# Kernel tuning notes

Measured on AMD Instinct MI355X. Metric: run time of the kernel, lower is better.

The kernel has to match this reference:

```python
import jax, jax.numpy as jnp
import numpy as np

B, L, C1, C2, K, K_IN = 4, 1024, 1024, 1024, 32, 32
BN_EPS = 1e-5


def _gated_bottleneck(x2d, conv_w, conv_b, gamma, beta, lin_w, lin_b):
    # x2d: (N, C1). Grouped 1x1 Conv1d with groups = C1//4: each group maps 4
    # input channels -> 1 output channel.
    n = x2d.shape[0]
    g = conv_w.shape[0]  # bottleneck = C1 // 4
    xc = jnp.einsum('ngf,gf->ng', x2d.reshape(n, g, 4), conv_w) + conv_b
    # BatchNorm1d in training mode: biased batch statistics over N (spatial dim is 1)
    mean = jnp.mean(xc, axis=0)
    var = jnp.mean((xc - mean) ** 2, axis=0)
    xn = (xc - mean) * jax.lax.rsqrt(var + BN_EPS) * gamma + beta
    xa = jax.nn.gelu(xn, approximate=False)  # torch nn.GELU default is exact
    return xa @ lin_w.T + lin_b  # (N, out_features)


def setup_inputs() -> dict:
    key = jax.random.key(0)
    ks = jax.random.split(key, 8)
    g = C1 // 4
    w_std = (2.0 / C2) ** 0.5  # kaiming_normal_ fan_in on (c1, c2)
    lin_std = (1.0 / g) ** 0.5
    return {
        'x': jax.random.normal(ks[0], (B, L, C1), jnp.float32),
        'weight': jax.random.normal(ks[1], (C1, C2), jnp.float32) * w_std,
        'bias': jnp.zeros((C2,), jnp.float32),
        'so_conv_w': jax.random.normal(ks[2], (g, 4), jnp.float32) * 0.5,
        'so_conv_b': jnp.zeros((g,), jnp.float32),
        'so_gamma': jnp.ones((g,), jnp.float32),
        'so_beta': jnp.zeros((g,), jnp.float32),
        'so_lin_w': jax.random.normal(ks[3], (C2, g), jnp.float32) * lin_std,
        'so_lin_b': jnp.zeros((C2,), jnp.float32),
        'si_conv_w': jax.random.normal(ks[4], (g, 4), jnp.float32) * 0.5,
        'si_conv_b': jnp.zeros((g,), jnp.float32),
        'si_gamma': jnp.ones((g,), jnp.float32),
        'si_beta': jnp.zeros((g,), jnp.float32),
        'si_lin_w': jax.random.normal(ks[5], (C1, g), jnp.float32) * lin_std,
        'si_lin_b': jnp.zeros((C1,), jnp.float32),
    }


def reference(x, weight, bias,
              so_conv_w, so_conv_b, so_gamma, so_beta, so_lin_w, so_lin_b,
              si_conv_w, si_conv_b, si_gamma, si_beta, si_lin_w, si_lin_b):
    b, l, c1 = x.shape
    c2 = weight.shape[1]
    x2d = x.reshape(b * l, c1)
    bi = jnp.arange(b)[:, None, None]
    li = jnp.arange(l)[None, :, None]

    # ---- output-sparse branch ----
    score_out = jax.nn.softmax(
        _gated_bottleneck(x2d, so_conv_w, so_conv_b, so_gamma, so_beta,
                          so_lin_w, so_lin_b).reshape(b, l, c2), axis=-1)
    s_v_out, s_i_out = jax.lax.top_k(score_out, K)  # (b,l,K)
    # x . W[:, idx]  ==  (x @ W) gathered at idx; avoids (b,l,c1,K) gather
    full = jnp.einsum('blc,co->blo', x, weight)  # (b,l,c2)
    out_k = jnp.take_along_axis(full, s_i_out, axis=-1) * s_v_out  # (b,l,K)
    out_branch = jnp.zeros((b, l, c2), x.dtype).at[bi, li, s_i_out].add(out_k)

    # ---- input-sparse branch ----
    score_in = jax.nn.softmax(
        _gated_bottleneck(x2d, si_conv_w, si_conv_b, si_gamma, si_beta,
                          si_lin_w, si_lin_b).reshape(b, l, c1), axis=-1)
    s_v_in, s_i_in = jax.lax.top_k(score_in, K_IN)  # (b,l,K_IN)
    x_gated = jnp.take_along_axis(x, s_i_in, axis=-1) * s_v_in  # (b,l,K_IN)
    # sum_k x_gated * W[idx[k], :]  ==  scatter(x_gated) @ W (topk idx unique);
    # avoids materializing (b,l,K_IN,c2) gathered weight rows.
    x_sparse = jnp.zeros((b, l, c1), x.dtype).at[bi, li, s_i_in].add(x_gated)
    in_branch = jnp.einsum('blc,co->blo', x_sparse, weight)

    return out_branch + in_branch + bias
```

## Files before the change

kernel.cpp:

```cpp
#include <hip/hip_runtime.h>
#include <hip/hip_fp16.h>
#include <math.h>


typedef __attribute__((ext_vector_type(8))) short short8;
typedef __attribute__((ext_vector_type(4))) float f32x4;

__device__ __forceinline__ unsigned int ford(float f) {
    unsigned int b = __float_as_uint(f);
    return (b & 0x80000000u) ? ~b : (b | 0x80000000u);
}

__global__ __launch_bounds__(256) void prep_k(
    const float* __restrict__ W,
    const float* __restrict__ so_lw, const float* __restrict__ si_lw,
    const float* __restrict__ x,
    const float* __restrict__ so_cw, const float* __restrict__ so_cb,
    const float* __restrict__ si_cw, const float* __restrict__ si_cb,
    __half* __restrict__ wT16, __half* __restrict__ W16,
    unsigned short* __restrict__ whl,
    float* __restrict__ xc, float* __restrict__ partials) {
    int bid = blockIdx.x;
    int t = threadIdx.x;
    if (bid < 1024) {
        __shared__ float tile[32][33];
        int c0 = (bid & 31) * 32, r0 = (bid >> 5) * 32;
        int tx = t & 31, ty = t >> 5;
#pragma unroll
        for (int i = 0; i < 32; i += 8) {
            float v = W[(size_t)(r0 + ty + i) * 1024 + c0 + tx];
            tile[ty + i][tx] = v;
            W16[(size_t)(r0 + ty + i) * 1024 + c0 + tx] = __float2half_rn(v);
        }
        __syncthreads();
#pragma unroll
        for (int i = 0; i < 32; i += 8)
            wT16[(size_t)(c0 + ty + i) * 1024 + r0 + tx] =
                __float2half_rn(tile[tx][ty + i]);
    } else if (bid < 1280) {
        int g = (bid - 1024) * 256 + t;
        int br = g >> 15;
        int rem = g & 32767;
        int ct = rem >> 9;
        int kt = (rem >> 6) & 7;
        int l  = rem & 63;
        int col = ct * 16 + (l & 15);
        int ks  = kt * 32 + (l >> 4) * 8;
        const float* lw = (br ? si_lw : so_lw) + (size_t)col * 256 + ks;
        float4 v0 = *(const float4*)lw;
        float4 v1 = *(const float4*)(lw + 4);
        unsigned hh[8], ll[8];
#pragma unroll
        for (int j = 0; j < 8; ++j) {
            float a = j < 4 ? (&v0.x)[j] : (&v1.x)[j - 4];
            unsigned b = __float_as_uint(a);
            unsigned rh = (b + 0x7FFFu + ((b >> 16) & 1u)) & 0xFFFF0000u;
            hh[j] = rh >> 16;
            float res = a - __uint_as_float(rh);
            unsigned c = __float_as_uint(res);
            unsigned rl = (c + 0x7FFFu + ((c >> 16) & 1u)) & 0xFFFF0000u;
            ll[j] = rl >> 16;
        }
        uint4 ph, pl;
        ph.x = hh[0] | (hh[1] << 16); ph.y = hh[2] | (hh[3] << 16);
        ph.z = hh[4] | (hh[5] << 16); ph.w = hh[6] | (hh[7] << 16);
        pl.x = ll[0] | (ll[1] << 16); pl.y = ll[2] | (ll[3] << 16);
        pl.z = ll[4] | (ll[5] << 16); pl.w = ll[6] | (ll[7] << 16);
        size_t base = (((((size_t)br * 2 + 0) * 64 + ct) * 8 + kt) * 64 + l) * 8;
        size_t hstride = (size_t)64 * 8 * 64 * 8;
        *(uint4*)&whl[base]           = ph;
        *(uint4*)&whl[base + hstride] = pl;
    } else {
        int g = t;
        int n0 = (bid - 1280) * 16;
        float4 wo = ((const float4*)so_cw)[g]; float bo = so_cb[g];
        float4 wi = ((const float4*)si_cw)[g]; float bi = si_cb[g];
        float so_s = 0.f, so_q = 0.f, si_s = 0.f, si_q = 0.f;
#pragma unroll
        for (int r = 0; r < 16; ++r) {
            int n = n0 + r;
            float4 xv = ((const float4*)x)[n * 256 + g];
            float co = fmaf(xv.x, wo.x, fmaf(xv.y, wo.y, fmaf(xv.z, wo.z, fmaf(xv.w, wo.w, bo))));
            float ci = fmaf(xv.x, wi.x, fmaf(xv.y, wi.y, fmaf(xv.z, wi.z, fmaf(xv.w, wi.w, bi))));
            xc[n * 256 + g] = co;
            xc[1048576 + n * 256 + g] = ci;
            so_s += co; so_q += co * co;
            si_s += ci; si_q += ci * ci;
        }
        int b = bid - 1280;
        partials[(b * 4 + 0) * 256 + g] = so_s;
        partials[(b * 4 + 1) * 256 + g] = so_q;
        partials[(b * 4 + 2) * 256 + g] = si_s;
        partials[(b * 4 + 3) * 256 + g] = si_q;
    }
}

__global__ __launch_bounds__(256) void stats_k(
    const float* __restrict__ partials,
    const float* __restrict__ g_so, const float* __restrict__ b_so,
    const float* __restrict__ g_si, const float* __restrict__ b_si,
    float* __restrict__ sc) {
    int g = threadIdx.x;
    int br = blockIdx.x;
    float s = 0.f, q = 0.f;
    for (int b = 0; b < 256; ++b) {
        s += partials[(b * 4 + br * 2 + 0) * 256 + g];
        q += partials[(b * 4 + br * 2 + 1) * 256 + g];
    }
    float mean = s * (1.f / 4096.f);
    float var  = q * (1.f / 4096.f) - mean * mean;
    float rstd = rsqrtf(var + 1e-5f);
    float gm = br ? g_si[g] : g_so[g];
    float bt = br ? b_si[g] : b_so[g];
    float scale = gm * rstd;
    sc[br * 512 + g]       = scale;
    sc[br * 512 + 256 + g] = fmaf(-mean, scale, bt);
}

__global__ __launch_bounds__(256) void gelusplit_k(
    const float* __restrict__ xc, const float* __restrict__ sc,
    unsigned short* __restrict__ xah, unsigned short* __restrict__ xal) {
    int s = blockIdx.x * 256 + threadIdx.x;
    int br  = s >> 17;
    int rem = s & 131071;
    int rtg = rem >> 9;
    int kt  = (rem >> 6) & 7;
    int l   = rem & 63;
    int row = rtg * 16 + (l & 15);
    int ks  = kt * 32 + (l >> 4) * 8;
    const float* xp  = xc + (size_t)br * 1048576 + (size_t)row * 256 + ks;
    const float* scp = sc + br * 512;
    float4 c0 = *(const float4*)xp;
    float4 c1 = *(const float4*)(xp + 4);
    float4 s0 = *(const float4*)(scp + ks);
    float4 s1 = *(const float4*)(scp + ks + 4);
    float4 h0 = *(const float4*)(scp + 256 + ks);
    float4 h1 = *(const float4*)(scp + 256 + ks + 4);
    unsigned hh[8], ll[8];
#pragma unroll
    for (int j = 0; j < 8; ++j) {
        float cv  = j < 4 ? (&c0.x)[j] : (&c1.x)[j - 4];
        float scl = j < 4 ? (&s0.x)[j] : (&s1.x)[j - 4];
        float shf = j < 4 ? (&h0.x)[j] : (&h1.x)[j - 4];
        float z = fmaf(cv, scl, shf);
        float a = 0.5f * z * (1.f + erff(z * 0.70710678f));
        unsigned b = __float_as_uint(a);
        unsigned rh = (b + 0x7FFFu + ((b >> 16) & 1u)) & 0xFFFF0000u;
        hh[j] = rh >> 16;
        float res = a - __uint_as_float(rh);
        unsigned cc = __float_as_uint(res);
        unsigned rl = (cc + 0x7FFFu + ((cc >> 16) & 1u)) & 0xFFFF0000u;
        ll[j] = rl >> 16;
    }
    uint4 ph, pl;
    ph.x = hh[0] | (hh[1] << 16); ph.y = hh[2] | (hh[3] << 16);
    ph.z = hh[4] | (hh[5] << 16); ph.w = hh[6] | (hh[7] << 16);
    pl.x = ll[0] | (ll[1] << 16); pl.y = ll[2] | (ll[3] << 16);
    pl.z = ll[4] | (ll[5] << 16); pl.w = ll[6] | (ll[7] << 16);
    *(uint4*)&xah[(size_t)s * 8] = ph;
    *(uint4*)&xal[(size_t)s * 8] = pl;
}

__global__ __launch_bounds__(256, 2) void logits_mfma2_k(
    const unsigned short* __restrict__ xah, const unsigned short* __restrict__ xal,
    const unsigned short* __restrict__ whl,
    const float* __restrict__ so_lb, const float* __restrict__ si_lb,
    float* __restrict__ logits) {
    int t = threadIdx.x;
    int bx = blockIdx.x;
    int n0 = bx * 64;
    int cb = blockIdx.y;
    int br = blockIdx.z;
    int wave = t >> 6, lane = t & 63;

    f32x4 acc[4][4];
#pragma unroll
    for (int ci = 0; ci < 4; ++ci)
#pragma unroll
        for (int rt = 0; rt < 4; ++rt) acc[ci][rt] = (f32x4){0.f, 0.f, 0.f, 0.f};

    const size_t hstride = (size_t)64 * 8 * 64 * 8;
#pragma unroll 2
    for (int kt = 0; kt < 8; ++kt) {
        short8 Ah[4], Al[4];
#pragma unroll
        for (int rt = 0; rt < 4; ++rt) {
            size_t aoff = (((size_t)br * 256 + bx * 4 + rt) * 8 + kt) * 512 +
                          (size_t)lane * 8;
            Ah[rt] = *(const short8*)&xah[aoff];
            Al[rt] = *(const short8*)&xal[aoff];
        }
#pragma unroll
        for (int ci = 0; ci < 4; ++ci) {
            int ctg = cb * 16 + wave * 4 + ci;
            size_t boff = ((((size_t)br * 2 + 0) * 64 + ctg) * 8 + kt) * 512 +
                          (size_t)lane * 8;
            short8 Wh = *(const short8*)&whl[boff];
            short8 Wl = *(const short8*)&whl[boff + hstride];
#pragma unroll
            for (int rt = 0; rt < 4; ++rt) {
                acc[ci][rt] = __builtin_amdgcn_mfma_f32_16x16x32_bf16(Ah[rt], Wh, acc[ci][rt], 0, 0, 0);
                acc[ci][rt] = __builtin_amdgcn_mfma_f32_16x16x32_bf16(Ah[rt], Wl, acc[ci][rt], 0, 0, 0);
                acc[ci][rt] = __builtin_amdgcn_mfma_f32_16x16x32_bf16(Al[rt], Wh, acc[ci][rt], 0, 0, 0);
                acc[ci][rt] = __builtin_amdgcn_mfma_f32_16x16x32_bf16(Al[rt], Wl, acc[ci][rt], 0, 0, 0);
            }
        }
    }

    const float* lb = br ? si_lb : so_lb;
#pragma unroll
    for (int ci = 0; ci < 4; ++ci) {
        int colg = cb * 256 + (wave * 4 + ci) * 16 + (lane & 15);
        float lbv = lb[colg];
#pragma unroll
        for (int rt = 0; rt < 4; ++rt) {
#pragma unroll
            for (int i = 0; i < 4; ++i) {
                int row = n0 + rt * 16 + (lane >> 4) * 4 + i;
                logits[((size_t)br * 4096 + row) * 1024 + colg] = acc[ci][rt][i] + lbv;
            }
        }
    }
}

__global__ __launch_bounds__(64) void topk_k(const float* __restrict__ logits,
                                             unsigned int* __restrict__ tidx,
                                             float* __restrict__ tval) {
    __shared__ unsigned int hist[256];
    __shared__ unsigned int wcnt;
    int lane = threadIdx.x;
    int rb = blockIdx.x;
    unsigned int* h = hist;

    const float4* lg = (const float4*)(logits + (size_t)rb * 1024);
    float v[16];
#pragma unroll
    for (int q = 0; q < 4; ++q) {
        float4 f = lg[q * 64 + lane];
        v[q * 4 + 0] = f.x; v[q * 4 + 1] = f.y;
        v[q * 4 + 2] = f.z; v[q * 4 + 3] = f.w;
    }
    float rmax = v[0];
#pragma unroll
    for (int i = 1; i < 16; ++i) rmax = fmaxf(rmax, v[i]);
#pragma unroll
    for (int s = 32; s; s >>= 1) rmax = fmaxf(rmax, __shfl_xor(rmax, s));
    float rsum = 0.f;
#pragma unroll
    for (int i = 0; i < 16; ++i) rsum += __expf(v[i] - rmax);
#pragma unroll
    for (int s = 32; s; s >>= 1) rsum += __shfl_xor(rsum, s);

    unsigned int kb[16];
#pragma unroll
    for (int i = 0; i < 16; ++i) kb[i] = ford(v[i]);

    unsigned inmask = 0xFFFFu;
    unsigned need = 32, prefix = 0, lasth = 0;
#pragma unroll
    for (int level = 0; level < 3; ++level) {
        int shift = 24 - level * 8;
        ((uint4*)h)[lane] = make_uint4(0u, 0u, 0u, 0u);
        __syncthreads();
#pragma unroll
        for (int i = 0; i < 16; ++i)
            if ((inmask >> i) & 1u) atomicAdd(&h[(kb[i] >> shift) & 0xFFu], 1u);
        __syncthreads();
        uint4 hv = ((const uint4*)h)[lane];
        unsigned sl = hv.x + hv.y + hv.z + hv.w;
        unsigned S = sl;
#pragma unroll
        for (int off = 1; off < 64; off <<= 1) {
            unsigned o = __shfl_down(S, off);
            if (lane + off < 64) S += o;
        }
        unsigned above = S - sl;
        unsigned cg3 = above + hv.w;
        unsigned cg2 = cg3 + hv.z;
        unsigned cg1 = cg2 + hv.y;
        unsigned cg0 = cg1 + hv.x;
        unsigned pack = 0;
        if      (cg3 >= need) pack = ((4u * lane + 3u) << 12) | cg3;
        else if (cg2 >= need) pack = ((4u * lane + 2u) << 12) | cg2;
        else if (cg1 >= need) pack = ((4u * lane + 1u) << 12) | cg1;
        else if (cg0 >= need) pack = ((4u * lane + 0u) << 12) | cg0;
#pragma unroll
        for (int s = 32; s; s >>= 1) {
            unsigned o = __shfl_xor(pack, s);
            pack = o > pack ? o : pack;
        }
        unsigned bstar = pack >> 12, cstar = pack & 0xFFFu;
        unsigned hstar = h[bstar];
        need -= (cstar - hstar);
        prefix = (prefix << 8) | bstar;
        lasth = hstar;
        unsigned nm = 0;
#pragma unroll
        for (int i = 0; i < 16; ++i)
            if (((inmask >> i) & 1u) && ((kb[i] >> shift) & 0xFFu) == bstar)
                nm |= 1u << i;
        inmask = nm;
        __syncthreads();
    }

    unsigned winmask = 0;
    if (lasth == need) {
        winmask = inmask;
    } else {
        unsigned avail = inmask;
        unsigned long long best = 0ULL;
#pragma unroll
        for (int i = 0; i < 16; ++i)
            if ((avail >> i) & 1u) {
                int j = (i >> 2) * 256 + lane * 4 + (i & 3);
                unsigned long long k64 =
                    ((unsigned long long)kb[i] << 32) | (unsigned int)(~j);
                best = k64 > best ? k64 : best;
            }
        for (unsigned k = 0; k < need; ++k) {
            unsigned long long w = best;
#pragma unroll
            for (int s = 32; s; s >>= 1) {
                unsigned long long o = __shfl_xor(w, s);
                if (o > w) w = o;
            }
            if (best == w) {
                unsigned long long nb = 0ULL;
#pragma unroll
                for (int i = 0; i < 16; ++i)
                    if ((avail >> i) & 1u) {
                        int j = (i >> 2) * 256 + lane * 4 + (i & 3);
                        unsigned long long k64 =
                            ((unsigned long long)kb[i] << 32) | (unsigned int)(~j);
                        if (k64 == w) { winmask |= 1u << i; avail &= ~(1u << i); }
                        else nb = k64 > nb ? k64 : nb;
                    }
                best = nb;
            }
        }
    }

    if (lane == 0) wcnt = 0;
#pragma unroll
    for (int i = 0; i < 16; ++i) {
        bool wn = ((kb[i] >> 8) > prefix) || ((winmask >> i) & 1u);
        if (wn) {
            unsigned slot = atomicAdd(&wcnt, 1u);
            int j = (i >> 2) * 256 + lane * 4 + (i & 3);
            tidx[(size_t)rb * 32 + slot] = (unsigned int)j;
            tval[(size_t)rb * 32 + slot] = __expf(v[i] - rmax) / rsum;
        }
    }
}

__global__ __launch_bounds__(256) void final16_k(
    const float* __restrict__ x, const __half* __restrict__ wT16,
    const __half* __restrict__ W16, const float* __restrict__ bias,
    const unsigned int* __restrict__ tidx, const float* __restrict__ tval,
    float* __restrict__ out) {
    int n = blockIdx.x, t = threadIdx.x, wave = t >> 6, lane = t & 63;
    __shared__ float xr[1024];
    __shared__ float dres[32];
    __shared__ unsigned int gidx[32]; __shared__ float gval[32];
    __shared__ unsigned int iidx[32]; __shared__ float ival[32];

    ((float4*)xr)[t] = ((const float4*)(x + (size_t)n * 1024))[t];
    if (t < 32) {
        gidx[t] = tidx[(size_t)n * 32 + t];
        gval[t] = tval[(size_t)n * 32 + t];
    } else if (t < 64) {
        int k = t - 32;
        iidx[k] = tidx[((size_t)4096 + n) * 32 + k];
        ival[k] = tval[((size_t)4096 + n) * 32 + k];
    }
    __syncthreads();

    if (t < 32) ival[t] *= xr[iidx[t]];

    const float4* xr4 = (const float4*)xr;
#pragma unroll
    for (int d8 = 0; d8 < 8; ++d8) {
        int d = wave * 8 + d8;
        const uint4* wrow = (const uint4*)(wT16 + (size_t)gidx[d] * 1024);
        float s = 0.f;
#pragma unroll
        for (int q = 0; q < 2; ++q) {
            int idx = q * 64 + lane;
            uint4 wv = wrow[idx];
            float4 xa = xr4[idx * 2];
            float4 xb = xr4[idx * 2 + 1];
            float2 f0 = __half22float2(*(const __half2*)&wv.x);
            float2 f1 = __half22float2(*(const __half2*)&wv.y);
            float2 f2 = __half22float2(*(const __half2*)&wv.z);
            float2 f3 = __half22float2(*(const __half2*)&wv.w);
            s += xa.x * f0.x + xa.y * f0.y + xa.z * f1.x + xa.w * f1.y +
                 xb.x * f2.x + xb.y * f2.y + xb.z * f3.x + xb.w * f3.y;
        }
#pragma unroll
        for (int sft = 32; sft; sft >>= 1) s += __shfl_xor(s, sft);
        if (lane == 0) dres[d] = s * gval[d];
    }
    __syncthreads();

    float4 acc = ((const float4*)bias)[t];
    for (int k = 0; k < 32; ++k) {
        float g = ival[k];
        unsigned int c = iidx[k];
        uint2 wv = ((const uint2*)(W16 + (size_t)c * 1024))[t];
        float2 f0 = __half22float2(*(const __half2*)&wv.x);
        float2 f1 = __half22float2(*(const __half2*)&wv.y);
        acc.x = fmaf(g, f0.x, acc.x); acc.y = fmaf(g, f0.y, acc.y);
        acc.z = fmaf(g, f1.x, acc.z); acc.w = fmaf(g, f1.y, acc.w);
    }
    ((float4*)xr)[t] = acc;
    __syncthreads();
    if (t < 32) xr[gidx[t]] += dres[t];
    __syncthreads();
    ((float4*)(out + (size_t)n * 1024))[t] = ((float4*)xr)[t];
}

extern "C" void kernel_launch(void* const* d_in, const int* in_sizes, int n_in,
                              void* d_out, int out_size, void* d_ws, size_t ws_size,
                              hipStream_t stream) {
    (void)in_sizes; (void)n_in; (void)out_size; (void)ws_size;
    const float* x        = (const float*)d_in[0];
    const float* W        = (const float*)d_in[1];
    const float* bias     = (const float*)d_in[2];
    const float* so_cw    = (const float*)d_in[3];
    const float* so_cb    = (const float*)d_in[4];
    const float* so_gm    = (const float*)d_in[5];
    const float* so_bt    = (const float*)d_in[6];
    const float* so_lw    = (const float*)d_in[7];
    const float* so_lb    = (const float*)d_in[8];
    const float* si_cw    = (const float*)d_in[9];
    const float* si_cb    = (const float*)d_in[10];
    const float* si_gm    = (const float*)d_in[11];
    const float* si_bt    = (const float*)d_in[12];
    const float* si_lw    = (const float*)d_in[13];
    const float* si_lb    = (const float*)d_in[14];
    float* out = (float*)d_out;

    float* ws       = (float*)d_ws;
    __half* wT16    = (__half*)ws;
    __half* W16     = (__half*)(ws + 524288);
    unsigned short* whl = (unsigned short*)(ws + 1048576);
    float* xc       = ws + 1572864;
    float* partials = ws + 3670016;
    float* sc       = ws + 3932160;
    float* logits   = ws + 3933184;
    unsigned int* tidx = (unsigned int*)(ws + 12321792);
    float* tval     = ws + 12583936;
    unsigned short* xah = (unsigned short*)(ws + 12977152);
    unsigned short* xal = (unsigned short*)(ws + 14025728);

    prep_k<<<1536, 256, 0, stream>>>(W, so_lw, si_lw, x, so_cw, so_cb, si_cw, si_cb,
                                     wT16, W16, whl, xc, partials);
    stats_k<<<2, 256, 0, stream>>>(partials, so_gm, so_bt, si_gm, si_bt, sc);
    gelusplit_k<<<1024, 256, 0, stream>>>(xc, sc, xah, xal);
    logits_mfma2_k<<<dim3(64, 4, 2), 256, 0, stream>>>(xah, xal, whl, so_lb, si_lb, logits);
    topk_k<<<8192, 64, 0, stream>>>(logits, tidx, tval);
    final16_k<<<4096, 256, 0, stream>>>(x, wT16, W16, bias, tidx, tval, out);
}
```

Measured before the change: 118.9 us.

## Fuse top-k selection into final kernel and drop low-low MFMA term

The separate top-k kernel is merged into the final gather kernel. Two waves per block each run the radix-select for one branch while the other two waves stage the x row into shared memory, so the top-k indices and values stay in LDS instead of going through global buffers and a second launch. The split-bf16 logits GEMM also drops the Al*Wl product, cutting MFMA work by a quarter at the cost of slightly lower logit precision, which could change top-k selection near ties.

```diff
diff --git a/kernel.cpp b/kernel.cpp
--- a/kernel.cpp
+++ b/kernel.cpp
@@ -202,7 +202,6 @@
                 acc[ci][rt] = __builtin_amdgcn_mfma_f32_16x16x32_bf16(Ah[rt], Wh, acc[ci][rt], 0, 0, 0);
                 acc[ci][rt] = __builtin_amdgcn_mfma_f32_16x16x32_bf16(Ah[rt], Wl, acc[ci][rt], 0, 0, 0);
                 acc[ci][rt] = __builtin_amdgcn_mfma_f32_16x16x32_bf16(Al[rt], Wh, acc[ci][rt], 0, 0, 0);
-                acc[ci][rt] = __builtin_amdgcn_mfma_f32_16x16x32_bf16(Al[rt], Wl, acc[ci][rt], 0, 0, 0);
             }
         }
     }
@@ -223,155 +222,150 @@
     }
 }
 
-__global__ __launch_bounds__(64) void topk_k(const float* __restrict__ logits,
-                                             unsigned int* __restrict__ tidx,
-                                             float* __restrict__ tval) {
-    __shared__ unsigned int hist[256];
-    __shared__ unsigned int wcnt;
-    int lane = threadIdx.x;
-    int rb = blockIdx.x;
-    unsigned int* h = hist;
-
-    const float4* lg = (const float4*)(logits + (size_t)rb * 1024);
-    float v[16];
-#pragma unroll
-    for (int q = 0; q < 4; ++q) {
-        float4 f = lg[q * 64 + lane];
-        v[q * 4 + 0] = f.x; v[q * 4 + 1] = f.y;
-        v[q * 4 + 2] = f.z; v[q * 4 + 3] = f.w;
-    }
-    float rmax = v[0];
-#pragma unroll
-    for (int i = 1; i < 16; ++i) rmax = fmaxf(rmax, v[i]);
-#pragma unroll
-    for (int s = 32; s; s >>= 1) rmax = fmaxf(rmax, __shfl_xor(rmax, s));
-    float rsum = 0.f;
-#pragma unroll
-    for (int i = 0; i < 16; ++i) rsum += __expf(v[i] - rmax);
-#pragma unroll
-    for (int s = 32; s; s >>= 1) rsum += __shfl_xor(rsum, s);
-
-    unsigned int kb[16];
-#pragma unroll
-    for (int i = 0; i < 16; ++i) kb[i] = ford(v[i]);
-
-    unsigned inmask = 0xFFFFu;
-    unsigned need = 32, prefix = 0, lasth = 0;
-#pragma unroll
-    for (int level = 0; level < 3; ++level) {
-        int shift = 24 - level * 8;
-        ((uint4*)h)[lane] = make_uint4(0u, 0u, 0u, 0u);
-        __syncthreads();
-#pragma unroll
-        for (int i = 0; i < 16; ++i)
-            if ((inmask >> i) & 1u) atomicAdd(&h[(kb[i] >> shift) & 0xFFu], 1u);
-        __syncthreads();
-        uint4 hv = ((const uint4*)h)[lane];
-        unsigned sl = hv.x + hv.y + hv.z + hv.w;
-        unsigned S = sl;
-#pragma unroll
-        for (int off = 1; off < 64; off <<= 1) {
-            unsigned o = __shfl_down(S, off);
-            if (lane + off < 64) S += o;
-        }
-        unsigned above = S - sl;
-        unsigned cg3 = above + hv.w;
-        unsigned cg2 = cg3 + hv.z;
-        unsigned cg1 = cg2 + hv.y;
-        unsigned cg0 = cg1 + hv.x;
-        unsigned pack = 0;
-        if      (cg3 >= need) pack = ((4u * lane + 3u) << 12) | cg3;
-        else if (cg2 >= need) pack = ((4u * lane + 2u) << 12) | cg2;
-        else if (cg1 >= need) pack = ((4u * lane + 1u) << 12) | cg1;
-        else if (cg0 >= need) pack = ((4u * lane + 0u) << 12) | cg0;
-#pragma unroll
-        for (int s = 32; s; s >>= 1) {
-            unsigned o = __shfl_xor(pack, s);
-            pack = o > pack ? o : pack;
-        }
-        unsigned bstar = pack >> 12, cstar = pack & 0xFFFu;
-        unsigned hstar = h[bstar];
-        need -= (cstar - hstar);
-        prefix = (prefix << 8) | bstar;
-        lasth = hstar;
-        unsigned nm = 0;
-#pragma unroll
-        for (int i = 0; i < 16; ++i)
-            if (((inmask >> i) & 1u) && ((kb[i] >> shift) & 0xFFu) == bstar)
-                nm |= 1u << i;
-        inmask = nm;
-        __syncthreads();
-    }
-
-    unsigned winmask = 0;
-    if (lasth == need) {
-        winmask = inmask;
-    } else {
-        unsigned avail = inmask;
-        unsigned long long best = 0ULL;
-#pragma unroll
-        for (int i = 0; i < 16; ++i)
-            if ((avail >> i) & 1u) {
-                int j = (i >> 2) * 256 + lane * 4 + (i & 3);
-                unsigned long long k64 =
-                    ((unsigned long long)kb[i] << 32) | (unsigned int)(~j);
-                best = k64 > best ? k64 : best;
-            }
-        for (unsigned k = 0; k < need; ++k) {
-            unsigned long long w = best;
-#pragma unroll
-            for (int s = 32; s; s >>= 1) {
-                unsigned long long o = __shfl_xor(w, s);
-                if (o > w) w = o;
-            }
-            if (best == w) {
-                unsigned long long nb = 0ULL;
-#pragma unroll
-                for (int i = 0; i < 16; ++i)
-                    if ((avail >> i) & 1u) {
-                        int j = (i >> 2) * 256 + lane * 4 + (i & 3);
-                        unsigned long long k64 =
-                            ((unsigned long long)kb[i] << 32) | (unsigned int)(~j);
-                        if (k64 == w) { winmask |= 1u << i; avail &= ~(1u << i); }
-                        else nb = k64 > nb ? k64 : nb;
-                    }
-                best = nb;
-            }
-        }
-    }
-
-    if (lane == 0) wcnt = 0;
-#pragma unroll
-    for (int i = 0; i < 16; ++i) {
-        bool wn = ((kb[i] >> 8) > prefix) || ((winmask >> i) & 1u);
-        if (wn) {
-            unsigned slot = atomicAdd(&wcnt, 1u);
-            int j = (i >> 2) * 256 + lane * 4 + (i & 3);
-            tidx[(size_t)rb * 32 + slot] = (unsigned int)j;
-            tval[(size_t)rb * 32 + slot] = __expf(v[i] - rmax) / rsum;
-        }
-    }
-}
-
-__global__ __launch_bounds__(256) void final16_k(
-    const float* __restrict__ x, const __half* __restrict__ wT16,
-    const __half* __restrict__ W16, const float* __restrict__ bias,
-    const unsigned int* __restrict__ tidx, const float* __restrict__ tval,
-    float* __restrict__ out) {
+__global__ __launch_bounds__(256) void topkfinal_k(
+    const float* __restrict__ logits, const float* __restrict__ x,
+    const __half* __restrict__ wT16, const __half* __restrict__ W16,
+    const float* __restrict__ bias, float* __restrict__ out) {
     int n = blockIdx.x, t = threadIdx.x, wave = t >> 6, lane = t & 63;
     __shared__ float xr[1024];
     __shared__ float dres[32];
     __shared__ unsigned int gidx[32]; __shared__ float gval[32];
     __shared__ unsigned int iidx[32]; __shared__ float ival[32];
-
-    ((float4*)xr)[t] = ((const float4*)(x + (size_t)n * 1024))[t];
-    if (t < 32) {
-        gidx[t] = tidx[(size_t)n * 32 + t];
-        gval[t] = tval[(size_t)n * 32 + t];
-    } else if (t < 64) {
-        int k = t - 32;
-        iidx[k] = tidx[((size_t)4096 + n) * 32 + k];
-        ival[k] = tval[((size_t)4096 + n) * 32 + k];
+    __shared__ unsigned int hist[2][256];
+    __shared__ unsigned int wcnt[2];
+
+    float v[16];
+    unsigned int kb[16];
+    float rmax = 0.f, rsum = 0.f;
+    unsigned inmask = 0xFFFFu, need = 32, prefix = 0, lasth = 0;
+
+    if (wave < 2) {
+        const float4* lg = (const float4*)(logits + ((size_t)wave * 4096 + n) * 1024);
+#pragma unroll
+        for (int q = 0; q < 4; ++q) {
+            float4 f = lg[q * 64 + lane];
+            v[q * 4 + 0] = f.x; v[q * 4 + 1] = f.y;
+            v[q * 4 + 2] = f.z; v[q * 4 + 3] = f.w;
+        }
+        rmax = v[0];
+#pragma unroll
+        for (int i = 1; i < 16; ++i) rmax = fmaxf(rmax, v[i]);
+#pragma unroll
+        for (int s = 32; s; s >>= 1) rmax = fmaxf(rmax, __shfl_xor(rmax, s));
+#pragma unroll
+        for (int i = 0; i < 16; ++i) rsum += __expf(v[i] - rmax);
+#pragma unroll
+        for (int s = 32; s; s >>= 1) rsum += __shfl_xor(rsum, s);
+#pragma unroll
+        for (int i = 0; i < 16; ++i) kb[i] = ford(v[i]);
+    } else {
+        int i = t - 128;
+        const float4* xrow = (const float4*)(x + (size_t)n * 1024);
+        ((float4*)xr)[i]       = xrow[i];
+        ((float4*)xr)[i + 128] = xrow[i + 128];
+    }
+
+    for (int level = 0; level < 3; ++level) {
+        int shift = 24 - level * 8;
+        if (wave < 2) ((uint4*)hist[wave])[lane] = make_uint4(0u, 0u, 0u, 0u);
+        __syncthreads();
+        if (wave < 2) {
+            unsigned int* h = hist[wave];
+#pragma unroll
+            for (int i = 0; i < 16; ++i)
+                if ((inmask >> i) & 1u) atomicAdd(&h[(kb[i] >> shift) & 0xFFu], 1u);
+        }
+        __syncthreads();
+        if (wave < 2) {
+            unsigned int* h = hist[wave];
+            uint4 hv = ((const uint4*)h)[lane];
+            unsigned sl = hv.x + hv.y + hv.z + hv.w;
+            unsigned S = sl;
+#pragma unroll
+            for (int off = 1; off < 64; off <<= 1) {
+                unsigned o = __shfl_down(S, off);
+                if (lane + off < 64) S += o;
+            }
+            unsigned above = S - sl;
+            unsigned cg3 = above + hv.w;
+            unsigned cg2 = cg3 + hv.z;
+            unsigned cg1 = cg2 + hv.y;
+            unsigned cg0 = cg1 + hv.x;
+            unsigned pack = 0;
+            if      (cg3 >= need) pack = ((4u * lane + 3u) << 12) | cg3;
+            else if (cg2 >= need) pack = ((4u * lane + 2u) << 12) | cg2;
+            else if (cg1 >= need) pack = ((4u * lane + 1u) << 12) | cg1;
+            else if (cg0 >= need) pack = ((4u * lane + 0u) << 12) | cg0;
+#pragma unroll
+            for (int s = 32; s; s >>= 1) {
+                unsigned o = __shfl_xor(pack, s);
+                pack = o > pack ? o : pack;
+            }
+            unsigned bstar = pack >> 12, cstar = pack & 0xFFFu;
+            unsigned hstar = h[bstar];
+            need -= (cstar - hstar);
+            prefix = (prefix << 8) | bstar;
+            lasth = hstar;
+            unsigned nm = 0;
+#pragma unroll
+            for (int i = 0; i < 16; ++i)
+                if (((inmask >> i) & 1u) && ((kb[i] >> shift) & 0xFFu) == bstar)
+                    nm |= 1u << i;
+            inmask = nm;
+        }
+        __syncthreads();
+    }
+
+    if (wave < 2) {
+        unsigned winmask = 0;
+        if (lasth == need) {
+            winmask = inmask;
+        } else {
+            unsigned avail = inmask;
+            unsigned long long best = 0ULL;
+#pragma unroll
+            for (int i = 0; i < 16; ++i)
+                if ((avail >> i) & 1u) {
+                    int j = (i >> 2) * 256 + lane * 4 + (i & 3);
+                    unsigned long long k64 =
+                        ((unsigned long long)kb[i] << 32) | (unsigned int)(~j);
+                    best = k64 > best ? k64 : best;
+                }
+            for (unsigned k = 0; k < need; ++k) {
+                unsigned long long w = best;
+#pragma unroll
+                for (int s = 32; s; s >>= 1) {
+                    unsigned long long o = __shfl_xor(w, s);
+                    if (o > w) w = o;
+                }
+                if (best == w) {
+                    unsigned long long nb = 0ULL;
+#pragma unroll
+                    for (int i = 0; i < 16; ++i)
+                        if ((avail >> i) & 1u) {
+                            int j = (i >> 2) * 256 + lane * 4 + (i & 3);
+                            unsigned long long k64 =
+                                ((unsigned long long)kb[i] << 32) | (unsigned int)(~j);
+                            if (k64 == w) { winmask |= 1u << i; avail &= ~(1u << i); }
+                            else nb = k64 > nb ? k64 : nb;
+                        }
+                    best = nb;
+                }
+            }
+        }
+        if (lane == 0) wcnt[wave] = 0;
+        unsigned int* oid = wave ? iidx : gidx;
+        float*        ovl = wave ? ival : gval;
+#pragma unroll
+        for (int i = 0; i < 16; ++i) {
+            bool wn = ((kb[i] >> 8) > prefix) || ((winmask >> i) & 1u);
+            if (wn) {
+                unsigned slot = atomicAdd(&wcnt[wave], 1u);
+                int j = (i >> 2) * 256 + lane * 4 + (i & 3);
+                oid[slot] = (unsigned int)j;
+                ovl[slot] = __expf(v[i] - rmax) / rsum;
+            }
+        }
     }
     __syncthreads();
 
@@ -448,16 +442,13 @@
     float* partials = ws + 3670016;
     float* sc       = ws + 3932160;
     float* logits   = ws + 3933184;
-    unsigned int* tidx = (unsigned int*)(ws + 12321792);
-    float* tval     = ws + 12583936;
-    unsigned short* xah = (unsigned short*)(ws + 12977152);
-    unsigned short* xal = (unsigned short*)(ws + 14025728);
+    unsigned short* xah = (unsigned short*)(ws + 12321792);
+    unsigned short* xal = (unsigned short*)(ws + 13370368);
 
     prep_k<<<1536, 256, 0, stream>>>(W, so_lw, si_lw, x, so_cw, so_cb, si_cw, si_cb,
                                      wT16, W16, whl, xc, partials);
     stats_k<<<2, 256, 0, stream>>>(partials, so_gm, so_bt, si_gm, si_bt, sc);
     gelusplit_k<<<1024, 256, 0, stream>>>(xc, sc, xah, xal);
     logits_mfma2_k<<<dim3(64, 4, 2), 256, 0, stream>>>(xah, xal, whl, so_lb, si_lb, logits);
-    topk_k<<<8192, 64, 0, stream>>>(logits, tidx, tval);
-    final16_k<<<4096, 256, 0, stream>>>(x, wT16, W16, bias, tidx, tval, out);
-}
+    topkfinal_k<<<4096, 256, 0, stream>>>(logits, x, wT16, W16, bias, out);
+}
```

New measurement: 111.4 us. 1.07x faster.
